# Kernel optimization log

Hardware: AMD Instinct MI355X
Metric: run time of the kernel (lower is better)

## Reference

```python
import jax, jax.numpy as jnp
import numpy as np

N_NODES = 1048576   # total nodes across the ragged batch
N_GRAPHS = 16384    # number of graphs (segments)
D_IN = 128
D = 128


def setup_inputs() -> dict:
    key = jax.random.key(0)
    ks = jax.random.split(key, 8)
    x = jax.random.normal(ks[0], (N_NODES, D_IN), jnp.float32)
    graph_ids = jnp.sort(jax.random.randint(ks[1], (N_NODES,), 0, N_GRAPHS, jnp.int32))
    s_in = 1.0 / np.sqrt(D_IN)
    s_d = 1.0 / np.sqrt(D)
    W_enc = jax.random.normal(ks[2], (D_IN, D), jnp.float32) * s_in
    b_enc = jnp.zeros((D,), jnp.float32)
    w_q1 = jax.random.normal(ks[3], (D,), jnp.float32) * s_d
    b_q1 = jnp.zeros((), jnp.float32)
    w_q2 = jax.random.normal(ks[4], (D,), jnp.float32) * s_d
    b_q2 = jnp.zeros((), jnp.float32)
    return {"x": x, "graph_ids": graph_ids, "W_enc": W_enc, "b_enc": b_enc,
            "w_q1": w_q1, "b_q1": b_q1, "w_q2": w_q2, "b_q2": b_q2}


def _attention_query(h, graph_ids, w, b):
    # per-node score -> segment-softmax -> weighted segment sum (== masked attention pooling)
    s = h @ w + b                                                   # [N]
    m = jax.ops.segment_max(s, graph_ids, num_segments=N_GRAPHS)    # [G]
    e = jnp.exp(s - m[graph_ids])                                   # [N]
    z = jax.ops.segment_sum(e, graph_ids, num_segments=N_GRAPHS)    # [G]
    a = e / jnp.maximum(z, 1e-12)[graph_ids]                        # [N]
    return jax.ops.segment_sum(a[:, None] * h, graph_ids, num_segments=N_GRAPHS)  # [G, D]


def reference(x, graph_ids, W_enc, b_enc, w_q1, b_q1, w_q2, b_q2):
    # encoder: per-node feature transform
    h = jax.nn.relu(x @ W_enc + b_enc)                              # [N, D]
    # keys: masked mean pooling == segment mean
    counts = jax.ops.segment_sum(jnp.ones((N_NODES,), h.dtype), graph_ids,
                                 num_segments=N_GRAPHS)             # [G]
    keys = jax.ops.segment_sum(h, graph_ids, num_segments=N_GRAPHS) / \
        jnp.maximum(counts, 1.0)[:, None]                           # [G, D]
    q1 = _attention_query(h, graph_ids, w_q1, b_q1)
    q2 = _attention_query(h, graph_ids, w_q2, b_q2)
    return (keys, q1, q2)
```

## Files before the change

### kernel.cpp

```cpp
#include <hip/hip_runtime.h>
#include <hip/hip_bf16.h>

#define NN 1048576
#define NG 16384
#define DD 128
#define GRIDB 512
#define WSTRIDE (GRIDB * 4)

typedef __bf16 bf16x8 __attribute__((ext_vector_type(8)));
typedef float f32x4 __attribute__((ext_vector_type(4)));

#define WAIT_VM8()  asm volatile("s_waitcnt vmcnt(8)" ::: "memory")
#define WAIT_VM0()  asm volatile("s_waitcnt vmcnt(0)" ::: "memory")
#define WAIT_LGKM() asm volatile("s_waitcnt lgkmcnt(0)" ::: "memory")

__device__ __forceinline__ unsigned short f2bf(float f) {
    unsigned int u = __float_as_uint(f);
    u += 0x7FFFu + ((u >> 16) & 1u);
    return (unsigned short)(u >> 16);
}

__global__ void prep_kernel(const int* __restrict__ gid, const float* __restrict__ W,
                            int* __restrict__ starts, unsigned short* __restrict__ Wl) {
    int t = blockIdx.x * 256 + threadIdx.x;
    if (t <= NG) {
        int lo = 0, hi = NN;
        while (lo < hi) { int mid = (lo + hi) >> 1; if (gid[mid] < t) lo = mid + 1; else hi = mid; }
        starts[t] = lo;
    }
    if (t < DD * DD) {
        int e = t & 7, l = (t >> 3) & 63, kk = (t >> 9) & 3, n = t >> 11;
        int k = kk * 32 + (l >> 4) * 8 + e;
        int col = n * 16 + (l & 15);
        Wl[t] = f2bf(W[k * DD + col]);
    }
}

__global__ __launch_bounds__(256, 2) void fused_kernel(
    const float* __restrict__ x, const int* __restrict__ starts,
    const unsigned short* __restrict__ Wl,
    const float* __restrict__ b_enc, const float* __restrict__ w_q1,
    const float* __restrict__ b_q1, const float* __restrict__ w_q2,
    const float* __restrict__ b_q2, float* __restrict__ out) {

    __shared__ float xbuf[4][2][16 * 128];
    __shared__ float bwq[DD][4];

    const int t = threadIdx.x, w = t >> 6, l = t & 63;
    const int lr = l & 15, lk = l >> 4;

    if (t < DD) { bwq[t][0] = b_enc[t]; bwq[t][1] = w_q1[t]; bwq[t][2] = w_q2[t]; bwq[t][3] = 0.f; }

    bf16x8 wfr[8][4];
#pragma unroll
    for (int n = 0; n < 8; ++n)
#pragma unroll
        for (int kk = 0; kk < 4; ++kk)
            wfr[n][kk] = *(const bf16x8*)&Wl[((n * 4 + kk) * 64 + l) * 8];

    const float bq1 = b_q1[0], bq2 = b_q2[0];
    __syncthreads();

    const int g0 = blockIdx.x * 4 + w;

    int ig = g0, ic0 = 0, is1 = 0;
    {
        ic0 = starts[ig]; is1 = starts[ig + 1];
        while (ic0 >= is1) {
            ig += WSTRIDE;
            if (ig >= NG) break;
            ic0 = starts[ig]; is1 = starts[ig + 1];
        }
    }

    auto issue_tile = [&](int bufIdx) {
        const int hi = is1 - 1;
#pragma unroll
        for (int inst = 0; inst < 8; ++inst) {
            const int rit = inst * 2 + (l >> 5);
            const int grow = min(ic0 + rit, hi);
            const int su = (l & 31) ^ (rit & 7);
            const float* src = x + (size_t)grow * DD + su * 4;
            float* dst = &xbuf[w][bufIdx][inst * 256];
            __builtin_amdgcn_global_load_lds(
                (const __attribute__((address_space(1))) void*)src,
                (__attribute__((address_space(3))) void*)dst, 16, 0, 0);
        }
    };
    auto adv_issue = [&]() {
        ic0 += 16;
        while (ic0 >= is1) {
            ig += WSTRIDE;
            if (ig >= NG) break;
            ic0 = starts[ig]; is1 = starts[ig + 1];
        }
    };

    int inflight = 0;
    if (ig < NG) { issue_tile(0); adv_issue(); inflight = 1; }
    if (ig < NG) { issue_tile(1); adv_issue(); inflight = 2; }
    int buf = 0;

    for (int cg = g0; cg < NG; cg += WSTRIDE) {
        const int cs0 = starts[cg], cs1 = starts[cg + 1];
        const int cnt = cs1 - cs0;

        float m1 = -1e30f, m2 = -1e30f, z1 = 0.f, z2 = 0.f;
        float ka[8], q1a[8], q2a[8];
#pragma unroll
        for (int n = 0; n < 8; ++n) { ka[n] = 0.f; q1a[n] = 0.f; q2a[n] = 0.f; }

        for (int cc0 = cs0; cc0 < cs1; cc0 += 16) {
            if (inflight >= 2) { WAIT_VM8(); } else { WAIT_VM0(); }

            const float* xb = &xbuf[w][buf][0];
            bf16x8 afr[4];
#pragma unroll
            for (int kk = 0; kk < 4; ++kk) {
                const int u0 = (kk * 8 + lk * 2)     ^ (lr & 7);
                const int u1 = (kk * 8 + lk * 2 + 1) ^ (lr & 7);
                const float4 f0 = *(const float4*)&xb[lr * 128 + u0 * 4];
                const float4 f1 = *(const float4*)&xb[lr * 128 + u1 * 4];
                bf16x8 a;
                a[0] = (__bf16)f0.x; a[1] = (__bf16)f0.y; a[2] = (__bf16)f0.z; a[3] = (__bf16)f0.w;
                a[4] = (__bf16)f1.x; a[5] = (__bf16)f1.y; a[6] = (__bf16)f1.z; a[7] = (__bf16)f1.w;
                afr[kk] = a;
            }
            WAIT_LGKM();
            inflight--;
            if (ig < NG) { issue_tile(buf); adv_issue(); inflight++; }
            buf ^= 1;

            f32x4 acc[8];
#pragma unroll
            for (int n = 0; n < 8; ++n) { acc[n][0] = 0.f; acc[n][1] = 0.f; acc[n][2] = 0.f; acc[n][3] = 0.f; }
#pragma unroll
            for (int n = 0; n < 8; ++n)
#pragma unroll
                for (int kk = 0; kk < 4; ++kk)
                    acc[n] = __builtin_amdgcn_mfma_f32_16x16x32_bf16(afr[kk], wfr[n][kk], acc[n], 0, 0, 0);

            float p1[4] = {0.f, 0.f, 0.f, 0.f}, p2[4] = {0.f, 0.f, 0.f, 0.f};
#pragma unroll
            for (int n = 0; n < 8; ++n) {
                const float4 bw = *(const float4*)bwq[n * 16 + lr];
#pragma unroll
                for (int j = 0; j < 4; ++j) {
                    float hv = fmaxf(acc[n][j] + bw.x, 0.f);
                    acc[n][j] = hv;
                    p1[j] += hv * bw.y;
                    p2[j] += hv * bw.z;
                }
            }
#pragma unroll
            for (int j = 0; j < 4; ++j)
#pragma unroll
                for (int d = 1; d < 16; d <<= 1) {
                    p1[j] += __shfl_xor(p1[j], d);
                    p2[j] += __shfl_xor(p2[j], d);
                }

            float v1[4], v2[4];
            float r1 = -1e30f, r2 = -1e30f;
#pragma unroll
            for (int j = 0; j < 4; ++j) {
                const bool vv = (cc0 + lk * 4 + j) < cs1;
                v1[j] = vv ? p1[j] + bq1 : -1e30f;
                v2[j] = vv ? p2[j] + bq2 : -1e30f;
                r1 = fmaxf(r1, v1[j]); r2 = fmaxf(r2, v2[j]);
            }
            r1 = fmaxf(r1, __shfl_xor(r1, 16)); r1 = fmaxf(r1, __shfl_xor(r1, 32));
            r2 = fmaxf(r2, __shfl_xor(r2, 16)); r2 = fmaxf(r2, __shfl_xor(r2, 32));

            const float nm1 = fmaxf(m1, r1), nm2 = fmaxf(m2, r2);
            const float sc1 = __expf(m1 - nm1), sc2 = __expf(m2 - nm2);
            float e1j[4], e2j[4];
            float cz1 = 0.f, cz2 = 0.f;
#pragma unroll
            for (int j = 0; j < 4; ++j) {
                e1j[j] = __expf(v1[j] - nm1);
                e2j[j] = __expf(v2[j] - nm2);
                cz1 += e1j[j]; cz2 += e2j[j];
            }
            cz1 += __shfl_xor(cz1, 16); cz1 += __shfl_xor(cz1, 32);
            cz2 += __shfl_xor(cz2, 16); cz2 += __shfl_xor(cz2, 32);
            z1 = z1 * sc1 + cz1; z2 = z2 * sc2 + cz2;
            m1 = nm1; m2 = nm2;

#pragma unroll
            for (int n = 0; n < 8; ++n) {
                float kaa = 0.f, q1aa = 0.f, q2aa = 0.f;
#pragma unroll
                for (int j = 0; j < 4; ++j) {
                    const float hv = acc[n][j];
                    const bool vv = (cc0 + lk * 4 + j) < cs1;
                    kaa  += vv ? hv : 0.f;
                    q1aa += e1j[j] * hv;
                    q2aa += e2j[j] * hv;
                }
                ka[n] += kaa;
                q1a[n] = q1a[n] * sc1 + q1aa;
                q2a[n] = q2a[n] * sc2 + q2aa;
            }
        }

#pragma unroll
        for (int n = 0; n < 8; ++n)
#pragma unroll
            for (int d = 16; d < 64; d <<= 1) {
                ka[n]  += __shfl_xor(ka[n],  d);
                q1a[n] += __shfl_xor(q1a[n], d);
                q2a[n] += __shfl_xor(q2a[n], d);
            }
        const float inv_cnt = 1.f / fmaxf((float)cnt, 1.f);
        const float iz1 = 1.f / fmaxf(z1, 1e-12f);
        const float iz2 = 1.f / fmaxf(z2, 1e-12f);
#pragma unroll
        for (int n2 = 0; n2 < 2; ++n2) {
            const int n = lk * 2 + n2;
            const int col = n * 16 + lr;
            out[(size_t)cg * DD + col]            = ka[n]  * inv_cnt;
            out[(size_t)(NG + cg) * DD + col]     = q1a[n] * iz1;
            out[(size_t)(2 * NG + cg) * DD + col] = q2a[n] * iz2;
        }
    }
}

extern "C" void kernel_launch(void* const* d_in, const int* in_sizes, int n_in,
                              void* d_out, int out_size, void* d_ws, size_t ws_size,
                              hipStream_t stream) {
    const float* x     = (const float*)d_in[0];
    const int*   gid   = (const int*)d_in[1];
    const float* W     = (const float*)d_in[2];
    const float* b_enc = (const float*)d_in[3];
    const float* w_q1  = (const float*)d_in[4];
    const float* b_q1  = (const float*)d_in[5];
    const float* w_q2  = (const float*)d_in[6];
    const float* b_q2  = (const float*)d_in[7];
    float* out = (float*)d_out;

    int* starts        = (int*)d_ws;
    unsigned short* Wl = (unsigned short*)((char*)d_ws + 131072);

    prep_kernel<<<65, 256, 0, stream>>>(gid, W, starts, Wl);
    fused_kernel<<<GRIDB, 256, 0, stream>>>(x, starts, Wl, b_enc, w_q1, b_q1, w_q2, b_q2, out);
}
```

Before: 190.5 us.

## Assign contiguous graph ranges per wave and keep bias/query weights in registers

Each wave now processes a contiguous block of 8 graphs instead of graphs strided across the whole grid. Consecutive nodes are then streamed from x contiguously, which should improve DRAM/TLB locality and prefetch continuity. The bias and query weight vectors move from shared memory into per-lane registers, which removes the LDS reads in the epilogue and the block-level barrier. The cost is 24 more VGPRs under the 2-waves launch bound, and load balance across waves now depends on the sizes of adjacent graphs.

```diff
diff --git a/kernel.cpp b/kernel.cpp
--- a/kernel.cpp
+++ b/kernel.cpp
@@ -5,7 +5,7 @@
 #define NG 16384
 #define DD 128
 #define GRIDB 512
-#define WSTRIDE (GRIDB * 4)
+#define GPW 8
 
 typedef __bf16 bf16x8 __attribute__((ext_vector_type(8)));
 typedef float f32x4 __attribute__((ext_vector_type(4)));
@@ -44,13 +44,10 @@
     const float* __restrict__ b_q2, float* __restrict__ out) {
 
     __shared__ float xbuf[4][2][16 * 128];
-    __shared__ float bwq[DD][4];
 
     const int t = threadIdx.x, w = t >> 6, l = t & 63;
     const int lr = l & 15, lk = l >> 4;
 
-    if (t < DD) { bwq[t][0] = b_enc[t]; bwq[t][1] = w_q1[t]; bwq[t][2] = w_q2[t]; bwq[t][3] = 0.f; }
-
     bf16x8 wfr[8][4];
 #pragma unroll
     for (int n = 0; n < 8; ++n)
@@ -58,19 +55,23 @@
         for (int kk = 0; kk < 4; ++kk)
             wfr[n][kk] = *(const bf16x8*)&Wl[((n * 4 + kk) * 64 + l) * 8];
 
+    float br[8], w1r[8], w2r[8];
+#pragma unroll
+    for (int n = 0; n < 8; ++n) {
+        br[n]  = b_enc[n * 16 + lr];
+        w1r[n] = w_q1[n * 16 + lr];
+        w2r[n] = w_q2[n * 16 + lr];
+    }
     const float bq1 = b_q1[0], bq2 = b_q2[0];
-    __syncthreads();
-
-    const int g0 = blockIdx.x * 4 + w;
-
-    int ig = g0, ic0 = 0, is1 = 0;
-    {
+
+    const int p = blockIdx.x * 4 + w;
+    const int gbeg = p * GPW, gend = gbeg + GPW;
+
+    int ig = gbeg;
+    int ic0 = starts[ig], is1 = starts[ig + 1];
+    while (ic0 >= is1) {
+        if (++ig >= gend) break;
         ic0 = starts[ig]; is1 = starts[ig + 1];
-        while (ic0 >= is1) {
-            ig += WSTRIDE;
-            if (ig >= NG) break;
-            ic0 = starts[ig]; is1 = starts[ig + 1];
-        }
     }
 
     auto issue_tile = [&](int bufIdx) {
@@ -90,18 +91,17 @@
     auto adv_issue = [&]() {
         ic0 += 16;
         while (ic0 >= is1) {
-            ig += WSTRIDE;
-            if (ig >= NG) break;
+            if (++ig >= gend) break;
             ic0 = starts[ig]; is1 = starts[ig + 1];
         }
     };
 
     int inflight = 0;
-    if (ig < NG) { issue_tile(0); adv_issue(); inflight = 1; }
-    if (ig < NG) { issue_tile(1); adv_issue(); inflight = 2; }
+    if (ig < gend) { issue_tile(0); adv_issue(); inflight = 1; }
+    if (ig < gend) { issue_tile(1); adv_issue(); inflight = 2; }
     int buf = 0;
 
-    for (int cg = g0; cg < NG; cg += WSTRIDE) {
+    for (int cg = gbeg; cg < gend; ++cg) {
         const int cs0 = starts[cg], cs1 = starts[cg + 1];
         const int cnt = cs1 - cs0;
 
@@ -128,7 +128,7 @@
             }
             WAIT_LGKM();
             inflight--;
-            if (ig < NG) { issue_tile(buf); adv_issue(); inflight++; }
+            if (ig < gend) { issue_tile(buf); adv_issue(); inflight++; }
             buf ^= 1;
 
             f32x4 acc[8];
@@ -143,13 +143,12 @@
             float p1[4] = {0.f, 0.f, 0.f, 0.f}, p2[4] = {0.f, 0.f, 0.f, 0.f};
 #pragma unroll
             for (int n = 0; n < 8; ++n) {
-                const float4 bw = *(const float4*)bwq[n * 16 + lr];
 #pragma unroll
                 for (int j = 0; j < 4; ++j) {
-                    float hv = fmaxf(acc[n][j] + bw.x, 0.f);
+                    float hv = fmaxf(acc[n][j] + br[n], 0.f);
                     acc[n][j] = hv;
-                    p1[j] += hv * bw.y;
-                    p2[j] += hv * bw.z;
+                    p1[j] += hv * w1r[n];
+                    p2[j] += hv * w2r[n];
                 }
             }
 #pragma unroll
```

Result: slower. 316.9 us (+66.4%).
